# Optimization experiments

Hardware: AMD Instinct MI355X
Metric: run time of the kernel (lower is better)

## Reference

```python
import jax, jax.numpy as jnp
import numpy as np

C = 1024
T = 2048
B = 8

def setup_inputs() -> dict:
    key = jax.random.key(0)
    ks = jax.random.split(key, 7)
    s = lambda fan_in: 1.0 / np.sqrt(fan_in)
    return {
        "x":     jax.random.normal(ks[0], (B, T, C), dtype=jnp.float32),
        "w_qkv": jax.random.uniform(ks[1], (C, 3 * C), jnp.float32, -s(C), s(C)),
        "w_proj": jax.random.uniform(ks[2], (C, C), jnp.float32, -s(C), s(C)),
        "w1":    jax.random.uniform(ks[3], (C, 2 * C), jnp.float32, -s(C), s(C)),
        "w2":    jax.random.uniform(ks[4], (2 * C, C), jnp.float32, -s(2 * C), s(2 * C)),
        "g1":    jnp.ones((C,), jnp.float32),
        "g2":    jnp.ones((C,), jnp.float32),
    }

def rmsnorm(x, g, eps=1e-6):
    return x * jax.lax.rsqrt(jnp.mean(x * x, axis=-1, keepdims=True) + eps) * g

def reference(x, w_qkv, w_proj, w1, w2, g1, g2):
    t = x.shape[1]
    # --- attention ---
    h = rmsnorm(x, g1)
    qkv = h @ w_qkv                               # [B,T,3C]
    q, k, v = jnp.split(qkv, 3, axis=-1)
    scores = jnp.einsum('bqc,bkc->bqk', q, k) * (C ** -0.5)  # [B,T,T]
    causal = jnp.triu(jnp.ones((t, t), dtype=bool), k=1)
    scores = jnp.where(causal, -jnp.inf, scores)
    attn = jax.nn.softmax(scores, axis=-1)
    x = x + (attn @ v) @ w_proj
    # --- ffn ---
    h = rmsnorm(x, g2)
    return x + (jax.nn.silu(h @ w1)) @ w2
```

## Files before the change

### kernel.cpp

```cpp
#include <hip/hip_runtime.h>
#include <hip/hip_bf16.h>
#include <stdint.h>


#define C_DIM 1024
#define T_DIM 2048
#define B_DIM 8

typedef float f32x4 __attribute__((ext_vector_type(4)));
typedef __bf16 bf16x8 __attribute__((ext_vector_type(8)));

typedef const __attribute__((address_space(1))) void gvoid_t;
typedef __attribute__((address_space(3))) void lvoid_t;

__device__ __forceinline__ void gload_lds16(const void* g, void* l) {
    __builtin_amdgcn_global_load_lds((gvoid_t*)g, (lvoid_t*)l, 16, 0, 0);
}

__device__ __forceinline__ unsigned short f2bf_bits(float f) {
    __hip_bfloat16 h = __float2bfloat16(f);
    return *reinterpret_cast<unsigned short*>(&h);
}

__device__ __forceinline__ void xcd_remap(int& bx, int& by, int& bz) {
    const int gx = gridDim.x, gy = gridDim.y;
    const int nwg = gx * gy * (int)gridDim.z;
    const int orig = bx + gx * (by + gy * bz);
    const int q = nwg >> 3, r = nwg & 7;
    const int xcd = orig & 7, pos = orig >> 3;
    const int neu = (xcd < r ? xcd * (q + 1) : r * (q + 1) + (xcd - r) * q) + pos;
    bx = neu % gx;
    const int t = neu / gx;
    by = t % gy;
    bz = t / gy;
}

#define BAR() do { __builtin_amdgcn_s_barrier(); __builtin_amdgcn_sched_barrier(0); } while(0)
#define VMCNT(n) do { asm volatile("s_waitcnt vmcnt(" #n ")" ::: "memory"); \
                      __builtin_amdgcn_sched_barrier(0); } while(0)

#define RDA(h, buf) do { \
    _Pragma("unroll") \
    for (int mf_ = 0; mf_ < 4; ++mf_) { \
        const char* p_ = lds + (buf)*32768 + wrb + (h)*8192 + mf_*2048; \
        aF[h][mf_][0] = *(const bf16x8*)(p_ + offk0); \
        aF[h][mf_][1] = *(const bf16x8*)(p_ + offk1); \
    } \
} while(0)

#define RDB(h, buf) do { \
    _Pragma("unroll") \
    for (int n2_ = 0; n2_ < 2; ++n2_) { \
        const char* p_ = lds + 65536 + (buf)*32768 + wcb + ((h)*2 + n2_)*2048; \
        bF[h][n2_][0] = *(const bf16x8*)(p_ + offk0); \
        bF[h][n2_][1] = *(const bf16x8*)(p_ + offk1); \
    } \
} while(0)

#define MM(Mh, Nh) do { \
    __builtin_amdgcn_s_setprio(1); \
    _Pragma("unroll") \
    for (int m4_ = 0; m4_ < 4; ++m4_) \
    _Pragma("unroll") \
    for (int n2_ = 0; n2_ < 2; ++n2_) \
    _Pragma("unroll") \
    for (int ks_ = 0; ks_ < 2; ++ks_) \
        acc[(Mh)*4 + m4_][(Nh)*2 + n2_] = __builtin_amdgcn_mfma_f32_16x16x32_bf16( \
            aF[Mh][m4_][ks_], bF[Nh][n2_][ks_], acc[(Mh)*4 + m4_][(Nh)*2 + n2_], 0, 0, 0); \
    __builtin_amdgcn_s_setprio(0); \
} while(0)

#define STA(buf, half, kt) do { \
    const int go_ = aoff + (half)*128*lda + (kt)*64; \
    char* lp_ = ldsw + (buf)*32768 + (half)*16384; \
    gload_lds16(A + go_,            lp_); \
    gload_lds16(A + go_ + 64*lda,   lp_ + 8192); \
} while(0)
#define STB(buf, half, kt) do { \
    const int go_ = boff + (half)*128*ldb + (kt)*64; \
    char* lp_ = ldsw + 65536 + (buf)*32768 + (half)*16384; \
    gload_lds16(Bt + go_,           lp_); \
    gload_lds16(Bt + go_ + 64*ldb,  lp_ + 8192); \
} while(0)

template<int EPI, int CMODE>
__global__ __launch_bounds__(512, 2)
void gemm256(const __hip_bfloat16* A, const __hip_bfloat16* Bt,
             void* Cout, const float* R, void* C2, void* C3,
             int K, int lda, int ldb, int ldc,
             long long sA, long long sB, long long sC, float scale)
{
    int bx = blockIdx.x, by = blockIdx.y, bz = blockIdx.z;
    xcd_remap(bx, by, bz);
    if constexpr (CMODE == 1) { if (bx > by) return; }

    const int tid  = threadIdx.x;
    const int lane = tid & 63, wave = tid >> 6;
    const int l15  = lane & 15, l4 = lane >> 4;
    const int wr   = wave >> 2, wc = wave & 3;
    const int m0   = by * 256, n0 = bx * 256;
    const int z    = bz;

    A  += (long long)z * sA;
    Bt += (long long)z * sB;

    __shared__ __align__(16) char lds_[131072];
    char* lds  = lds_;
    char* ldsw = lds_ + wave * 1024;

    int kmax = K;
    if constexpr (CMODE == 2) { int km = m0 + 256; kmax = km < K ? km : K; }
    const int NT = kmax >> 6, niter = NT >> 1;

    const int offk0 = l15 * 128 + (((l4)     ^ (l15 & 7)) << 4);
    const int offk1 = l15 * 128 + (((4 + l4) ^ (l15 & 7)) << 4);
    const int wrb = wr * 16384, wcb = wc * 8192;

    const int rowq  = tid >> 3;
    const int sslot = (tid & 7) ^ (rowq & 7);
    const int aoff  = (m0 + rowq) * lda + sslot * 8;
    const int boff  = (n0 + rowq) * ldb + sslot * 8;

    f32x4 acc[8][4];
#pragma unroll
    for (int i = 0; i < 8; ++i)
#pragma unroll
        for (int j = 0; j < 4; ++j) acc[i][j] = (f32x4){0.f, 0.f, 0.f, 0.f};
    bf16x8 aF[2][4][2], bF[2][2][2];

    STA(0, 0, 0); STA(0, 1, 0); STB(0, 0, 0); STB(0, 1, 0);
    STA(1, 0, 1); STA(1, 1, 1);
    VMCNT(4);
    BAR();
    RDA(0, 0); RDB(0, 0);

    for (int it = 0; it < niter; ++it) {
        const int t1 = 2 * it + 1;
        const int s0 = (2 * it + 2) % NT, s1 = (2 * it + 3) % NT;
        RDB(1, 0); STB(1, 0, t1); BAR(); MM(0, 0); BAR();
        RDA(1, 0); STB(1, 1, t1); BAR(); MM(0, 1); VMCNT(4); BAR();
        RDA(0, 1); STA(0, 0, s0); BAR(); MM(1, 0); VMCNT(2); BAR();
        RDB(0, 1); STA(0, 1, s0); BAR(); MM(1, 1); BAR();
        RDB(1, 1); RDA(1, 1); STB(0, 0, s0); BAR(); MM(0, 0); BAR();
        STB(0, 1, s0); BAR(); MM(0, 1); VMCNT(4); BAR();
        RDA(0, 0); STA(1, 0, s1); BAR(); MM(1, 0); VMCNT(2); BAR();
        RDB(0, 0); STA(1, 1, s1); BAR(); MM(1, 1); BAR();
    }

    asm volatile("s_waitcnt vmcnt(0)" ::: "memory");

    const long long cbase = (long long)z * sC;
#pragma unroll
    for (int mf = 0; mf < 8; ++mf) {
        const int rbase = m0 + wr * 128 + mf * 16 + l4 * 4;
#pragma unroll
        for (int nf = 0; nf < 4; ++nf) {
            const int col = n0 + wc * 64 + nf * 16 + l15;
#pragma unroll
            for (int r = 0; r < 4; ++r) {
                const float v = acc[mf][nf][r];
                const int row = rbase + r;
                if constexpr (EPI == 6) {
                    const int seg = col >> 10, ncol = col & 1023;
                    if (seg == 0) {
                        ((__hip_bfloat16*)Cout)[(long long)row * 1024 + ncol] =
                            __float2bfloat16(v);
                    } else if (seg == 1) {
                        ((__hip_bfloat16*)C2)[(long long)row * 1024 + ncol] =
                            __float2bfloat16(v);
                    } else {
                        const int b = row >> 11, t = row & 2047;
                        ((__hip_bfloat16*)C3)[((long long)b * C_DIM + ncol) * T_DIM + t] =
                            __float2bfloat16(v);
                    }
                } else {
                    const long long idx = cbase + (long long)row * ldc + col;
                    if constexpr (EPI == 0) {
                        ((__hip_bfloat16*)Cout)[idx] = __float2bfloat16(v);
                    } else if constexpr (EPI == 2) {
                        ((float*)Cout)[idx] = v + R[idx];
                    } else if constexpr (EPI == 3) {
                        const float s = v / (1.f + __expf(-v));
                        ((__hip_bfloat16*)Cout)[idx] = __float2bfloat16(s);
                    } else {
                        ((__hip_bfloat16*)Cout)[idx] = __float2bfloat16(v * scale);
                    }
                }
            }
        }
    }
}

__global__ __launch_bounds__(256)
void rmsnorm_kernel(const float* __restrict__ x, const float* __restrict__ g,
                    __hip_bfloat16* __restrict__ out)
{
    const long long row = blockIdx.x;
    const int tid = threadIdx.x;
    const float4 v = ((const float4*)(x + row * C_DIM))[tid];
    float ss = v.x * v.x + v.y * v.y + v.z * v.z + v.w * v.w;
#pragma unroll
    for (int off = 32; off; off >>= 1) ss += __shfl_xor(ss, off);
    __shared__ float red[4];
    if ((tid & 63) == 0) red[tid >> 6] = ss;
    __syncthreads();
    ss = red[0] + red[1] + red[2] + red[3];
    const float sc = rsqrtf(ss * (1.0f / C_DIM) + 1e-6f);
    const float4 gv = ((const float4*)g)[tid];
    ushort4 u;
    u.x = f2bf_bits(v.x * sc * gv.x);
    u.y = f2bf_bits(v.y * sc * gv.y);
    u.z = f2bf_bits(v.z * sc * gv.z);
    u.w = f2bf_bits(v.w * sc * gv.w);
    *(ushort4*)(out + row * C_DIM + tid * 4) = u;
}

__global__ __launch_bounds__(256)
void softmax_causal(__hip_bfloat16* __restrict__ SP)
{
    const int i = blockIdx.x, b = blockIdx.y;
    __hip_bfloat16* row = SP + ((long long)b * T_DIM + i) * T_DIM;
    const int tid = threadIdx.x;
    const int jbase = tid * 8;

    uint4 raw = ((const uint4*)row)[tid];
    float v[8];
    const unsigned w[4] = {raw.x, raw.y, raw.z, raw.w};
#pragma unroll
    for (int c = 0; c < 4; ++c) {
        unsigned lo = w[c] << 16;
        unsigned hi = w[c] & 0xFFFF0000u;
        v[2 * c]     = __uint_as_float(lo);
        v[2 * c + 1] = __uint_as_float(hi);
    }
#pragma unroll
    for (int e = 0; e < 8; ++e)
        if (jbase + e > i) v[e] = -1e30f;

    float m = v[0];
#pragma unroll
    for (int e = 1; e < 8; ++e) m = fmaxf(m, v[e]);
#pragma unroll
    for (int off = 32; off; off >>= 1) m = fmaxf(m, __shfl_xor(m, off));
    __shared__ float redm[4], reds[4];
    if ((tid & 63) == 0) redm[tid >> 6] = m;
    __syncthreads();
    m = fmaxf(fmaxf(redm[0], redm[1]), fmaxf(redm[2], redm[3]));

    float e8[8];
    float s = 0.f;
#pragma unroll
    for (int e = 0; e < 8; ++e) { e8[e] = __expf(v[e] - m); s += e8[e]; }
#pragma unroll
    for (int off = 32; off; off >>= 1) s += __shfl_xor(s, off);
    if ((tid & 63) == 0) reds[tid >> 6] = s;
    __syncthreads();
    s = reds[0] + reds[1] + reds[2] + reds[3];
    const float inv = 1.f / s;

    uint4 outw;
    unsigned o[4];
#pragma unroll
    for (int c = 0; c < 4; ++c) {
        unsigned lo = f2bf_bits(e8[2 * c] * inv);
        unsigned hi = f2bf_bits(e8[2 * c + 1] * inv);
        o[c] = lo | (hi << 16);
    }
    outw.x = o[0]; outw.y = o[1]; outw.z = o[2]; outw.w = o[3];
    ((uint4*)row)[tid] = outw;
}

__global__ __launch_bounds__(256)
void wcast_t(const float* __restrict__ in, __hip_bfloat16* __restrict__ out,
             int K, int N)
{
    __shared__ float t[32][33];
    const int n0 = blockIdx.x * 32, k0 = blockIdx.y * 32;
    const int tx = threadIdx.x, ty = threadIdx.y;
#pragma unroll
    for (int r = ty; r < 32; r += 8)
        t[r][tx] = in[(long long)(k0 + r) * N + n0 + tx];
    __syncthreads();
#pragma unroll
    for (int r = ty; r < 32; r += 8)
        out[(long long)(n0 + r) * K + k0 + tx] = __float2bfloat16(t[tx][r]);
}

extern "C" void kernel_launch(void* const* d_in, const int* in_sizes, int n_in,
                              void* d_out, int out_size, void* d_ws, size_t ws_size,
                              hipStream_t stream)
{
    const float* x      = (const float*)d_in[0];
    const float* w_qkv  = (const float*)d_in[1];
    const float* w_proj = (const float*)d_in[2];
    const float* w1     = (const float*)d_in[3];
    const float* w2     = (const float*)d_in[4];
    const float* g1     = (const float*)d_in[5];
    const float* g2     = (const float*)d_in[6];
    float* out = (float*)d_out;
    char* ws = (char*)d_ws;

    const size_t SP_off = 0;
    const size_t h_off  = 0;
    const size_t u_off  = 0;
    const size_t q_off  = 67108864ull;
    const size_t k_off  = 100663296ull;
    const size_t vT_off = 134217728ull;
    const size_t wq_off = 167772160ull;
    const size_t wp_off = wq_off + 6291456ull;
    const size_t w1_off = wp_off + 2097152ull;
    const size_t w2_off = w1_off + 4194304ull;
    const size_t NEED   = w2_off + 4194304ull;

    if (ws_size < NEED) return;

    auto bf = [&](size_t off) { return (__hip_bfloat16*)(ws + off); };

    wcast_t<<<dim3(96, 32), dim3(32, 8), 0, stream>>>(w_qkv,  bf(wq_off), 1024, 3072);
    wcast_t<<<dim3(32, 32), dim3(32, 8), 0, stream>>>(w_proj, bf(wp_off), 1024, 1024);
    wcast_t<<<dim3(64, 32), dim3(32, 8), 0, stream>>>(w1,     bf(w1_off), 1024, 2048);
    wcast_t<<<dim3(32, 64), dim3(32, 8), 0, stream>>>(w2,     bf(w2_off), 2048, 1024);

    rmsnorm_kernel<<<16384, 256, 0, stream>>>(x, g1, bf(h_off));

    gemm256<6, 0><<<dim3(12, 64, 1), 512, 0, stream>>>(
        bf(h_off), bf(wq_off), bf(q_off), nullptr, bf(k_off), bf(vT_off),
        1024, 1024, 1024, 1024, 0, 0, 0, 1.f);

    gemm256<4, 1><<<dim3(8, 8, 8), 512, 0, stream>>>(
        bf(q_off), bf(k_off), bf(SP_off), nullptr, nullptr, nullptr,
        1024, 1024, 1024, 2048,
        (long long)T_DIM * C_DIM, (long long)T_DIM * C_DIM, (long long)T_DIM * T_DIM,
        0.03125f);

    softmax_causal<<<dim3(2048, 8), 256, 0, stream>>>(bf(SP_off));

    gemm256<0, 2><<<dim3(4, 8, 8), 512, 0, stream>>>(
        bf(SP_off), bf(vT_off), bf(k_off) , nullptr, nullptr, nullptr,
        2048, 2048, 2048, 1024,
        (long long)T_DIM * T_DIM, (long long)C_DIM * T_DIM, (long long)T_DIM * C_DIM,
        1.f);

    gemm256<2, 0><<<dim3(4, 64, 1), 512, 0, stream>>>(
        bf(k_off) , bf(wp_off), out, x, nullptr, nullptr,
        1024, 1024, 1024, 1024, 0, 0, 0, 1.f);

    rmsnorm_kernel<<<16384, 256, 0, stream>>>(out, g2, bf(q_off));

    gemm256<3, 0><<<dim3(8, 64, 1), 512, 0, stream>>>(
        bf(q_off), bf(w1_off), bf(u_off), nullptr, nullptr, nullptr,
        1024, 1024, 1024, 2048, 0, 0, 0, 1.f);

    gemm256<2, 0><<<dim3(4, 64, 1), 512, 0, stream>>>(
        bf(u_off), bf(w2_off), out, (const float*)out, nullptr, nullptr,
        2048, 2048, 2048, 1024, 0, 0, 0, 1.f);
}
```

Before: 585.7 us.

## Reschedule GEMM main loop with single A-fragment buffer and reordered prefetches

Restructures the 8-phase software pipeline of the bf16 MFMA GEMM. A fragments are now single-buffered instead of double-buffered, which cuts register use. The global→LDS stage issues and the LDS reads are reordered across the MFMA phases, and the number of vmcnt waits drops to two per iteration. The aim is to keep two waves per SIMD with lower register pressure and fewer stalls. The catch is that LDS reads now sit directly before their MFMAs with less latency hiding, and the new ordering has to keep the buffers consistent.

```diff
diff --git a/kernel.cpp b/kernel.cpp
--- a/kernel.cpp
+++ b/kernel.cpp
@@ -39,21 +39,21 @@
 #define VMCNT(n) do { asm volatile("s_waitcnt vmcnt(" #n ")" ::: "memory"); \
                       __builtin_amdgcn_sched_barrier(0); } while(0)
 
-#define RDA(h, buf) do { \
+#define RDA(buf, hq) do { \
     _Pragma("unroll") \
     for (int mf_ = 0; mf_ < 4; ++mf_) { \
-        const char* p_ = lds + (buf)*32768 + wrb + (h)*8192 + mf_*2048; \
-        aF[h][mf_][0] = *(const bf16x8*)(p_ + offk0); \
-        aF[h][mf_][1] = *(const bf16x8*)(p_ + offk1); \
+        const char* p_ = lds + (buf)*32768 + wrb + (hq)*8192 + mf_*2048; \
+        aF[mf_][0] = *(const bf16x8*)(p_ + offk0); \
+        aF[mf_][1] = *(const bf16x8*)(p_ + offk1); \
     } \
 } while(0)
 
-#define RDB(h, buf) do { \
+#define RDB(buf, nh) do { \
     _Pragma("unroll") \
     for (int n2_ = 0; n2_ < 2; ++n2_) { \
-        const char* p_ = lds + 65536 + (buf)*32768 + wcb + ((h)*2 + n2_)*2048; \
-        bF[h][n2_][0] = *(const bf16x8*)(p_ + offk0); \
-        bF[h][n2_][1] = *(const bf16x8*)(p_ + offk1); \
+        const char* p_ = lds + 65536 + (buf)*32768 + wcb + ((nh)*2 + n2_)*2048; \
+        bF[nh][n2_][0] = *(const bf16x8*)(p_ + offk0); \
+        bF[nh][n2_][1] = *(const bf16x8*)(p_ + offk1); \
     } \
 } while(0)
 
@@ -66,7 +66,7 @@
     _Pragma("unroll") \
     for (int ks_ = 0; ks_ < 2; ++ks_) \
         acc[(Mh)*4 + m4_][(Nh)*2 + n2_] = __builtin_amdgcn_mfma_f32_16x16x32_bf16( \
-            aF[Mh][m4_][ks_], bF[Nh][n2_][ks_], acc[(Mh)*4 + m4_][(Nh)*2 + n2_], 0, 0, 0); \
+            aF[m4_][ks_], bF[Nh][n2_][ks_], acc[(Mh)*4 + m4_][(Nh)*2 + n2_], 0, 0, 0); \
     __builtin_amdgcn_s_setprio(0); \
 } while(0)
 
@@ -126,25 +126,36 @@
     for (int i = 0; i < 8; ++i)
 #pragma unroll
         for (int j = 0; j < 4; ++j) acc[i][j] = (f32x4){0.f, 0.f, 0.f, 0.f};
-    bf16x8 aF[2][4][2], bF[2][2][2];
-
-    STA(0, 0, 0); STA(0, 1, 0); STB(0, 0, 0); STB(0, 1, 0);
-    STA(1, 0, 1); STA(1, 1, 1);
+    bf16x8 aF[4][2], bF[2][2][2];
+
+    STB(0, 0, 0); STA(0, 0, 0); STA(0, 1, 0); STB(0, 1, 0);
+    STB(1, 0, 1); STA(1, 0, 1);
     VMCNT(4);
     BAR();
-    RDA(0, 0); RDB(0, 0);
 
     for (int it = 0; it < niter; ++it) {
         const int t1 = 2 * it + 1;
-        const int s0 = (2 * it + 2) % NT, s1 = (2 * it + 3) % NT;
-        RDB(1, 0); STB(1, 0, t1); BAR(); MM(0, 0); BAR();
-        RDA(1, 0); STB(1, 1, t1); BAR(); MM(0, 1); VMCNT(4); BAR();
-        RDA(0, 1); STA(0, 0, s0); BAR(); MM(1, 0); VMCNT(2); BAR();
-        RDB(0, 1); STA(0, 1, s0); BAR(); MM(1, 1); BAR();
-        RDB(1, 1); RDA(1, 1); STB(0, 0, s0); BAR(); MM(0, 0); BAR();
-        STB(0, 1, s0); BAR(); MM(0, 1); VMCNT(4); BAR();
-        RDA(0, 0); STA(1, 0, s1); BAR(); MM(1, 0); VMCNT(2); BAR();
-        RDB(0, 0); STA(1, 1, s1); BAR(); MM(1, 1); BAR();
+        const int s2 = (2 * it + 2) % NT, s3 = (2 * it + 3) % NT;
+        STA(1, 1, t1); STB(1, 1, t1);
+        RDA(0, 0); RDB(0, 0);
+        BAR(); MM(0, 0); BAR();
+        RDB(0, 1);
+        BAR(); MM(0, 1); BAR();
+        STB(0, 0, s2);
+        RDA(0, 1);
+        BAR(); MM(1, 0); BAR();
+        STA(0, 0, s2);
+        BAR(); MM(1, 1); VMCNT(4); BAR();
+        STA(0, 1, s2); STB(0, 1, s2);
+        RDA(1, 0); RDB(1, 0);
+        BAR(); MM(0, 0); BAR();
+        RDB(1, 1);
+        BAR(); MM(0, 1); BAR();
+        STB(1, 0, s3);
+        RDA(1, 1);
+        BAR(); MM(1, 0); BAR();
+        STA(1, 0, s3);
+        BAR(); MM(1, 1); VMCNT(4); BAR();
     }
 
     asm volatile("s_waitcnt vmcnt(0)" ::: "memory");
```

Result: no change. 591.1 us (+0.9%).

## Restructure GEMM main loop into a coarse double-buffered pipeline with fewer barriers

Applied to the files above, without the earlier changes.

Replaces the fine-grained 8-step interleaved schedule, which had a barrier around every MFMA quarter, with a coarser double-buffered loop. Each iteration issues one full stage load of A and B tiles per buffer and keeps two LDS-read fragment sets (aP/aQ, bL/bH) so reads overlap the MFMA quarters. There are only two wait-plus-barrier points per iteration. It also drops the wrap-around modulo prefetches past the end of K. The cost is that each stage now waits on vmcnt(0) before moving on, so fewer global loads stay in flight and latency hiding may be shallower.

```diff
diff --git a/kernel.cpp b/kernel.cpp
--- a/kernel.cpp
+++ b/kernel.cpp
@@ -39,25 +39,25 @@
 #define VMCNT(n) do { asm volatile("s_waitcnt vmcnt(" #n ")" ::: "memory"); \
                       __builtin_amdgcn_sched_barrier(0); } while(0)
 
-#define RDA(h, buf) do { \
+#define RD_A(dst, buf, hq) do { \
     _Pragma("unroll") \
     for (int mf_ = 0; mf_ < 4; ++mf_) { \
-        const char* p_ = lds + (buf)*32768 + wrb + (h)*8192 + mf_*2048; \
-        aF[h][mf_][0] = *(const bf16x8*)(p_ + offk0); \
-        aF[h][mf_][1] = *(const bf16x8*)(p_ + offk1); \
+        const char* p_ = lds + (buf)*32768 + wrb + (hq)*8192 + mf_*2048; \
+        dst[mf_][0] = *(const bf16x8*)(p_ + offk0); \
+        dst[mf_][1] = *(const bf16x8*)(p_ + offk1); \
     } \
 } while(0)
 
-#define RDB(h, buf) do { \
+#define RD_B(dst, buf, nh) do { \
     _Pragma("unroll") \
     for (int n2_ = 0; n2_ < 2; ++n2_) { \
-        const char* p_ = lds + 65536 + (buf)*32768 + wcb + ((h)*2 + n2_)*2048; \
-        bF[h][n2_][0] = *(const bf16x8*)(p_ + offk0); \
-        bF[h][n2_][1] = *(const bf16x8*)(p_ + offk1); \
+        const char* p_ = lds + 65536 + (buf)*32768 + wcb + ((nh)*2 + n2_)*2048; \
+        dst[n2_][0] = *(const bf16x8*)(p_ + offk0); \
+        dst[n2_][1] = *(const bf16x8*)(p_ + offk1); \
     } \
 } while(0)
 
-#define MM(Mh, Nh) do { \
+#define MMQ(aS, bS, Mh, Nh) do { \
     __builtin_amdgcn_s_setprio(1); \
     _Pragma("unroll") \
     for (int m4_ = 0; m4_ < 4; ++m4_) \
@@ -66,7 +66,7 @@
     _Pragma("unroll") \
     for (int ks_ = 0; ks_ < 2; ++ks_) \
         acc[(Mh)*4 + m4_][(Nh)*2 + n2_] = __builtin_amdgcn_mfma_f32_16x16x32_bf16( \
-            aF[Mh][m4_][ks_], bF[Nh][n2_][ks_], acc[(Mh)*4 + m4_][(Nh)*2 + n2_], 0, 0, 0); \
+            aS[m4_][ks_], bS[n2_][ks_], acc[(Mh)*4 + m4_][(Nh)*2 + n2_], 0, 0, 0); \
     __builtin_amdgcn_s_setprio(0); \
 } while(0)
 
@@ -82,6 +82,7 @@
     gload_lds16(Bt + go_,           lp_); \
     gload_lds16(Bt + go_ + 64*ldb,  lp_ + 8192); \
 } while(0)
+#define STAGE4(buf, kt) do { STA(buf,0,kt); STA(buf,1,kt); STB(buf,0,kt); STB(buf,1,kt); } while(0)
 
 template<int EPI, int CMODE>
 __global__ __launch_bounds__(512, 2)
@@ -126,25 +127,35 @@
     for (int i = 0; i < 8; ++i)
 #pragma unroll
         for (int j = 0; j < 4; ++j) acc[i][j] = (f32x4){0.f, 0.f, 0.f, 0.f};
-    bf16x8 aF[2][4][2], bF[2][2][2];
-
-    STA(0, 0, 0); STA(0, 1, 0); STB(0, 0, 0); STB(0, 1, 0);
-    STA(1, 0, 1); STA(1, 1, 1);
-    VMCNT(4);
+    bf16x8 aP[4][2], aQ[4][2], bL[2][2], bH[2][2];
+
+    STAGE4(0, 0);
+    STAGE4(1, 1);
+    VMCNT(8);
     BAR();
-    RDA(0, 0); RDB(0, 0);
+    RD_A(aP, 0, 0);
+    RD_B(bL, 0, 0);
 
     for (int it = 0; it < niter; ++it) {
-        const int t1 = 2 * it + 1;
-        const int s0 = (2 * it + 2) % NT, s1 = (2 * it + 3) % NT;
-        RDB(1, 0); STB(1, 0, t1); BAR(); MM(0, 0); BAR();
-        RDA(1, 0); STB(1, 1, t1); BAR(); MM(0, 1); VMCNT(4); BAR();
-        RDA(0, 1); STA(0, 0, s0); BAR(); MM(1, 0); VMCNT(2); BAR();
-        RDB(0, 1); STA(0, 1, s0); BAR(); MM(1, 1); BAR();
-        RDB(1, 1); RDA(1, 1); STB(0, 0, s0); BAR(); MM(0, 0); BAR();
-        STB(0, 1, s0); BAR(); MM(0, 1); VMCNT(4); BAR();
-        RDA(0, 0); STA(1, 0, s1); BAR(); MM(1, 0); VMCNT(2); BAR();
-        RDB(0, 0); STA(1, 1, s1); BAR(); MM(1, 1); BAR();
+        const int t0 = 2 * it, t1 = 2 * it + 1;
+        RD_B(bH, 0, 1);            MMQ(aP, bL, 0, 0);
+        RD_A(aQ, 0, 1);            MMQ(aP, bH, 0, 1);
+                                   MMQ(aQ, bL, 1, 0);
+        VMCNT(0); BAR();
+        if (t0 + 2 < NT) STAGE4(0, t0 + 2);
+        RD_A(aP, 1, 0);
+        RD_B(bL, 1, 0);
+                                   MMQ(aQ, bH, 1, 1);
+        RD_B(bH, 1, 1);            MMQ(aP, bL, 0, 0);
+        RD_A(aQ, 1, 1);            MMQ(aP, bH, 0, 1);
+                                   MMQ(aQ, bL, 1, 0);
+        VMCNT(0); BAR();
+        if (t1 + 2 < NT) STAGE4(1, t1 + 2);
+        if (it + 1 < niter) {
+            RD_A(aP, 0, 0);
+            RD_B(bL, 0, 0);
+        }
+                                   MMQ(aQ, bH, 1, 1);
     }
 
     asm volatile("s_waitcnt vmcnt(0)" ::: "memory");
```

After: 569.6 us. 1.03x faster.
